# Optimization experiments

Hardware: AMD Instinct MI355X
Metric: run time of the kernel (lower is better)

Reference implementation:

```python
import jax, jax.numpy as jnp
import numpy as np
from jax import lax

B, N, H, D = 4, 384, 8, 5          # graphs, nodes/graph, heads, max multi-hop dist
NE, E_TOT, DH, L = 2048, 8192, 256, 10  # edges/graph, total real edges, d_hidden, curve samples
N_SPATIAL, N_EDGE_DIST = 64, 128


def _bn(x, g, b):
    # eval-mode BatchNorm1d (running_mean=0, running_var=1): affine only
    return x * g + b


def _conv1d(x, w):
    # x: [E, C, L], w: [O, I, 3], SAME padding, stride 1
    return lax.conv_general_dilated(x, w, (1,), 'SAME',
                                    dimension_numbers=('NCH', 'OIH', 'NCH'))


def setup_inputs() -> dict:
    key = jax.random.key(0)
    ks = iter(jax.random.split(key, 64))
    nrm = lambda shape, s=0.02: jax.random.normal(next(ks), shape, jnp.float32) * s
    std = 0.02 / np.sqrt(12.0)  # init_params with n_layer=12 for Linear weights
    inp = {}
    inp['attn_bias'] = jax.random.normal(next(ks), (B, N + 1, N + 1), jnp.float32)
    inp['spatial_pos'] = jax.random.randint(next(ks), (B, N, N), 0, N_SPATIAL)
    inp['d2_dist'] = jax.random.normal(next(ks), (B, N, N, 32), jnp.float32)
    inp['a3_dist'] = jax.random.normal(next(ks), (B, N, N, 32), jnp.float32)
    inp['edge_data'] = jax.random.normal(next(ks), (E_TOT, L, 7), jnp.float32)
    inp['edge_path'] = jax.random.randint(next(ks), (B, N, N, D), 0, NE + 1)
    inp['edge_padding_mask'] = jnp.zeros((B, NE), bool)  # all real edges
    inp['src'] = jax.random.randint(next(ks), (E_TOT,), 0, B * N)
    inp['dst'] = jax.random.randint(next(ks), (E_TOT,), 0, B * N)
    inp['node_data'] = jax.random.normal(next(ks), (B * N, DH), jnp.float32)
    # --- parameters ---
    inp['spatial_emb'] = nrm((N_SPATIAL, H)).at[0].set(0.0)  # padding_idx=0
    inp['t_virtual'] = nrm((1, H))
    inp['w_d2'] = nrm((H, 32), std); inp['b_d2'] = jnp.zeros((H,), jnp.float32)
    inp['w_a3'] = nrm((H, 32), std); inp['b_a3'] = jnp.zeros((H,), jnp.float32)
    inp['cw1'] = nrm((64, 7, 3), std);  inp['cg1'] = jnp.ones((64,));  inp['cb1'] = jnp.zeros((64,))
    inp['cw2'] = nrm((128, 64, 3), std); inp['cg2'] = jnp.ones((128,)); inp['cb2'] = jnp.zeros((128,))
    inp['cw3'] = nrm((256, 128, 3), std); inp['cg3'] = jnp.ones((256,)); inp['cb3'] = jnp.zeros((256,))
    inp['cw_out'] = nrm((H, 256), std)
    # _EdgeConv (UV-Net style): proj Linear(d_hidden->H), MLP(H->64->H), BN, GIN eps
    inp['wp'] = nrm((H, DH), std); inp['bp'] = jnp.zeros((H,))
    inp['w1'] = nrm((64, H), std); inp['b1'] = jnp.zeros((64,))
    inp['g1'] = jnp.ones((64,)); inp['bb1'] = jnp.zeros((64,))
    inp['w2'] = nrm((H, 64), std); inp['b2'] = jnp.zeros((H,))
    inp['g_out'] = jnp.ones((H,)); inp['bb_out'] = jnp.zeros((H,))
    inp['eps'] = jnp.zeros((), jnp.float32)
    inp['edge_dis_w'] = nrm((N_EDGE_DIST * H * H, 1))
    return inp


def reference(attn_bias, spatial_pos, d2_dist, a3_dist, edge_data, edge_path,
              edge_padding_mask, src, dst, node_data, spatial_emb, t_virtual,
              w_d2, b_d2, w_a3, b_a3, cw1, cg1, cb1, cw2, cg2, cb2, cw3, cg3, cb3,
              cw_out, wp, bp, w1, b1, g1, bb1, w2, b2, g_out, bb_out, eps, edge_dis_w):
    gab = jnp.repeat(attn_bias[:, None], H, axis=1)            # [B,H,N+1,N+1]
    spb = spatial_emb[spatial_pos]                              # [B,N,N,H]
    d2b = d2_dist @ w_d2.T + b_d2                               # [B,N,N,H]
    a3b = a3_dist @ w_a3.T + b_a3                               # [B,N,N,H]
    # CurveEncoder on per-edge curve samples
    x = jnp.transpose(edge_data, (0, 2, 1))                     # [E,7,L]
    x = jax.nn.leaky_relu(_bn(_conv1d(x, cw1), cg1[:, None], cb1[:, None]))
    x = jax.nn.leaky_relu(_bn(_conv1d(x, cw2), cg2[:, None], cb2[:, None]))
    x = jax.nn.leaky_relu(_bn(_conv1d(x, cw3), cg3[:, None], cb3[:, None]))
    ef = jnp.mean(x, axis=-1) @ cw_out.T                        # [E,H]
    # _EdgeConv: combine endpoint node features with edge features
    proj = node_data @ wp.T + bp                                # [B*N,H]
    h = (1.0 + eps) * ef + proj[src] + proj[dst]
    h = jax.nn.relu(_bn(h @ w1.T + b1, g1, bb1)) @ w2.T + b2
    edge_out = jax.nn.relu(_bn(h, g_out, bb_out))               # [E,H]
    # scatter real-edge features into padded table (row NE stays zero = padding)
    valid = (~edge_padding_mask).reshape(-1)                    # [B*NE]
    gidx = jnp.maximum(jnp.cumsum(valid) - 1, 0)
    vals = jnp.where(valid[:, None], edge_out[gidx], 0.0).reshape(B, NE, H)
    edge_feature = jnp.zeros((B, NE + 1, H), edge_out.dtype).at[:, :NE].set(vals)
    # gather along multi-hop paths, per-distance head mixing (bmm), normalize
    ep = edge_path.reshape(B, N * N * D)
    edge_input = jax.vmap(lambda f, p: f[p])(edge_feature, ep)  # [B,N*N*D,H]
    edge_input = edge_input.reshape(B, N, N, D, H)
    wdis = edge_dis_w.reshape(-1, H, H)[:D]                     # [D,H,H]
    edge_input = jnp.einsum('bijdh,dhk->bijdk', edge_input, wdis)
    sp = jnp.where(spatial_pos == 0, 1, spatial_pos)
    sp = jnp.where(sp > 1, sp - 1, sp)
    sp = jnp.clip(sp, 0, D)
    edge_bias = edge_input.sum(-2) / sp[..., None].astype(edge_input.dtype)
    inner = spb + d2b + a3b + edge_bias                         # [B,N,N,H]
    gab = gab.at[:, :, 1:, 1:].add(jnp.transpose(inner, (0, 3, 1, 2)))
    t = t_virtual.reshape(1, H, 1)
    gab = gab.at[:, :, 1:, 0].add(t)
    gab = gab.at[:, :, 0, :].add(t)
    return gab + attn_bias[:, None]
```

## Files before the change

kernel.cpp:

```cpp
#include <hip/hip_runtime.h>

#define NB    4
#define NNODE 384
#define NH    8
#define ND    5
#define NEDGE 2048
#define NEP1  2049
#define ETOT  8192
#define DHID  256
#define NP1   385
#define SQ1   (NP1*NP1)
#define NPOS  98304
#define NPOS2 (NPOS + 2)

typedef __attribute__((ext_vector_type(8)))  short short8;
typedef __attribute__((ext_vector_type(16))) float float16;

__device__ __forceinline__ unsigned short f2bf(float f) {
    union { float f; unsigned int u; } v; v.f = f;
    unsigned int u = v.u;
    return (unsigned short)((u + 0x7FFFu + ((u >> 16) & 1u)) >> 16);
}
__device__ __forceinline__ unsigned pkbf(float a, float b) {
    return (unsigned)f2bf(a) | ((unsigned)f2bf(b) << 16);
}
__device__ __forceinline__ short8 mk8(unsigned a, unsigned b, unsigned c, unsigned d) {
    union { unsigned u[4]; short8 s; } x; x.u[0]=a; x.u[1]=b; x.u[2]=c; x.u[3]=d; return x.s;
}
__device__ __forceinline__ float leaky(float v) { return v > 0.f ? v : 0.01f * v; }
__device__ __forceinline__ float16 zero16() {
    float16 z;
#pragma unroll
    for (int i = 0; i < 16; ++i) z[i] = 0.f;
    return z;
}
__device__ __forceinline__ void gl_lds16(const void* g, void* l) {
    __builtin_amdgcn_global_load_lds(
        (const __attribute__((address_space(1))) unsigned int*)g,
        (__attribute__((address_space(3))) unsigned int*)l,
        16, 0, 0);
}

__global__ __launch_bounds__(256) void prep_kernel(
    const float* __restrict__ cw1, const float* __restrict__ cw2, const float* __restrict__ cw3,
    const float* __restrict__ cw_out,
    const float* __restrict__ node_data, const float* __restrict__ wp, const float* __restrict__ bp,
    unsigned short* __restrict__ W1f, unsigned short* __restrict__ W2f, unsigned short* __restrict__ W3f,
    unsigned short* __restrict__ Wof,
    float* __restrict__ proj, float* __restrict__ edge_feature)
{
    int gid = blockIdx.x * 256 + threadIdx.x;
    if (gid < 98304) {
        int j = gid & 7, lane = (gid >> 3) & 63, blk = gid >> 9;
        int ks = blk & 7, tp = (blk >> 3) % 3, mt = blk / 24;
        int oc = mt * 32 + (lane & 31);
        int ic = ks * 16 + (lane >> 5) * 8 + j;
        W3f[gid] = f2bf(cw3[(oc * 128 + ic) * 3 + tp]);
    } else if (gid < 122880) {
        int f = gid - 98304;
        int j = f & 7, lane = (f >> 3) & 63, blk = f >> 9;
        int ks = blk & 3, tp = (blk >> 2) % 3, mt = blk / 12;
        int oc = mt * 32 + (lane & 31);
        int ic = ks * 16 + (lane >> 5) * 8 + j;
        W2f[f] = f2bf(cw2[(oc * 64 + ic) * 3 + tp]);
    } else if (gid < 124928) {
        int f = gid - 122880;
        int j = f & 7, lane = (f >> 3) & 63, blk = f >> 9;
        int ks = blk & 1, mt = blk >> 1;
        int oc = mt * 32 + (lane & 31);
        int k = ks * 16 + (lane >> 5) * 8 + j;
        int tp = k >> 3, c = k & 7;
        float v = (tp < 3 && c < 7) ? cw1[oc * 21 + c * 3 + tp] : 0.f;
        W1f[f] = f2bf(v);
    } else if (gid < 137216) {
        int f = gid - 124928;
        int v = f >> 3, h = f & 7;
        const float* nd = node_data + (size_t)v * DHID;
        const float* ww = wp + h * DHID;
        float acc = bp[h];
#pragma unroll 4
        for (int c = 0; c < DHID; c += 4)
            acc += nd[c]*ww[c] + nd[c+1]*ww[c+1] + nd[c+2]*ww[c+2] + nd[c+3]*ww[c+3];
        proj[f] = acc;
    } else if (gid < 137248) {
        int f = gid - 137216;
        int b = f >> 3, h = f & 7;
        edge_feature[((size_t)b * NEP1 + NEDGE) * NH + h] = 0.f;
    } else if (gid < 145440) {
        int f = gid - 137248;
        int j = f & 7, lane = (f >> 3) & 63, g = f >> 9;
        int m = lane & 31;
        int k = g * 16 + (lane >> 5) * 8 + j;
        Wof[f] = (m < 8) ? f2bf(cw_out[m * 256 + k]) : (unsigned short)0;
    }
}

#define X0_GROWS 8
__global__ __launch_bounds__(256) void pack_kernel(
    const float* __restrict__ edge_data,
    unsigned short* __restrict__ X0buf, unsigned short* __restrict__ X1buf,
    unsigned short* __restrict__ X2buf)
{
    int gid = blockIdx.x * 256 + threadIdx.x;
    const int NX0 = (NPOS + 2 * X0_GROWS) * 8;
    if (gid < NX0) {
        int row = gid >> 3, ch = gid & 7;
        int pos = row - X0_GROWS;
        unsigned short v = 0;
        if (pos >= 0 && pos < NPOS && ch < 7) {
            int pm = pos % 12;
            if (pm >= 1 && pm <= 10)
                v = f2bf(edge_data[(size_t)(pos / 12) * 70 + (pm - 1) * 7 + ch]);
        }
        X0buf[gid] = v;
    } else if (gid < NX0 + 128) {
        int f = gid - NX0;
        int p = f >> 5, rest = f & 31;
        int row = (rest >> 4) ? (NPOS + 1) : 0, col = rest & 15;
        X1buf[((size_t)p * NPOS2 + row) * 16 + col] = 0;
    } else if (gid < NX0 + 128 + 256) {
        int f = gid - NX0 - 128;
        int p = f >> 5, rest = f & 31;
        int row = (rest >> 4) ? (NPOS + 1) : 0, col = rest & 15;
        X2buf[((size_t)p * NPOS2 + row) * 16 + col] = 0;
    }
}

__global__ __launch_bounds__(256, 4) void conv1_kernel(
    const unsigned short* __restrict__ X0, const unsigned short* __restrict__ W1f,
    const float* __restrict__ cg1, const float* __restrict__ cb1,
    unsigned short* __restrict__ X1)
{
    const int t = threadIdx.x, wv = t >> 6, lane = t & 63;
    const int q = lane >> 5, n = lane & 31;
    const int pos = blockIdx.x * 128 + wv * 32 + n;

    float16 acc0 = zero16(), acc1 = zero16();
#pragma unroll
    for (int ks = 0; ks < 2; ++ks) {
        short8 b  = *(const short8*)(X0 + (pos - 1 + 2 * ks + q) * 8);
        short8 a0 = *(const short8*)(W1f + ((0 * 2 + ks) * 64 + lane) * 8);
        short8 a1 = *(const short8*)(W1f + ((1 * 2 + ks) * 64 + lane) * 8);
        acc0 = __builtin_amdgcn_mfma_f32_32x32x16_bf16(a0, b, acc0, 0, 0, 0);
        acc1 = __builtin_amdgcn_mfma_f32_32x32x16_bf16(a1, b, acc1, 0, 0, 0);
    }
    int pm = pos % 12;
    bool valid = (pm != 0) && (pm != 11);
#pragma unroll
    for (int mt = 0; mt < 2; ++mt) {
        const float16& acc = mt ? acc1 : acc0;
#pragma unroll
        for (int r2 = 0; r2 < 4; ++r2) {
            int oc0 = mt * 32 + 8 * r2 + 4 * q;
            float4 g4 = *(const float4*)(cg1 + oc0);
            float4 b4 = *(const float4*)(cb1 + oc0);
            unsigned short uu[4];
            uu[0] = valid ? f2bf(leaky(acc[r2*4+0] * g4.x + b4.x)) : (unsigned short)0;
            uu[1] = valid ? f2bf(leaky(acc[r2*4+1] * g4.y + b4.y)) : (unsigned short)0;
            uu[2] = valid ? f2bf(leaky(acc[r2*4+2] * g4.z + b4.z)) : (unsigned short)0;
            uu[3] = valid ? f2bf(leaky(acc[r2*4+3] * g4.w + b4.w)) : (unsigned short)0;
            uint2 pk; pk.x = uu[0] | ((unsigned)uu[1] << 16); pk.y = uu[2] | ((unsigned)uu[3] << 16);
            *(uint2*)(void*)(X1 + ((size_t)(oc0 >> 4) * NPOS2 + pos + 1) * 16 + (oc0 & 15)) = pk;
        }
    }
}

__global__ __launch_bounds__(256, 3) void conv2_kernel(
    const unsigned short* __restrict__ X1, const unsigned short* __restrict__ W2f,
    const float* __restrict__ cg2, const float* __restrict__ cb2,
    unsigned short* __restrict__ X2)
{
    __shared__ __align__(16) unsigned short sB[2][1568];
    const int t = threadIdx.x, wv = t >> 6, lane = t & 63;
    const int q = lane >> 5, n = lane & 31;
    const int base = blockIdx.x * 96;
    const int cbase = (wv < 3) ? wv * 64 : 132;

    gl_lds16(X1 + ((size_t)0 * NPOS2 + base) * 16 + (cbase + lane) * 8,
             &sB[0][cbase * 8]);

    float16 acc[3];
#pragma unroll
    for (int nt = 0; nt < 3; ++nt) acc[nt] = zero16();

    __syncthreads();

#pragma unroll
    for (int ks = 0; ks < 4; ++ks) {
        if (ks < 3)
            gl_lds16(X1 + ((size_t)(ks + 1) * NPOS2 + base) * 16 + (cbase + lane) * 8,
                     &sB[(ks + 1) & 1][cbase * 8]);
        const unsigned short* bb = sB[ks & 1];
#pragma unroll
        for (int tp = 0; tp < 3; ++tp) {
            short8 a = *(const short8*)(W2f + (((wv * 3 + tp) * 4 + ks) * 64 + lane) * 8);
#pragma unroll
            for (int nt = 0; nt < 3; ++nt) {
                short8 b = *(const short8*)(bb + (nt * 32 + n + tp) * 16 + q * 8);
                acc[nt] = __builtin_amdgcn_mfma_f32_32x32x16_bf16(a, b, acc[nt], 0, 0, 0);
            }
        }
        __syncthreads();
    }

#pragma unroll
    for (int nt = 0; nt < 3; ++nt) {
        int pos = base + nt * 32 + n;
        int pm = pos % 12;
        bool valid = (pm != 0) && (pm != 11);
#pragma unroll
        for (int r2 = 0; r2 < 4; ++r2) {
            int oc0 = wv * 32 + 8 * r2 + 4 * q;
            float4 g4 = *(const float4*)(cg2 + oc0);
            float4 b4 = *(const float4*)(cb2 + oc0);
            unsigned short uu[4];
            uu[0] = valid ? f2bf(leaky(acc[nt][r2*4+0] * g4.x + b4.x)) : (unsigned short)0;
            uu[1] = valid ? f2bf(leaky(acc[nt][r2*4+1] * g4.y + b4.y)) : (unsigned short)0;
            uu[2] = valid ? f2bf(leaky(acc[nt][r2*4+2] * g4.z + b4.z)) : (unsigned short)0;
            uu[3] = valid ? f2bf(leaky(acc[nt][r2*4+3] * g4.w + b4.w)) : (unsigned short)0;
            uint2 pk; pk.x = uu[0] | ((unsigned)uu[1] << 16); pk.y = uu[2] | ((unsigned)uu[3] << 16);
            *(uint2*)(void*)(X2 + ((size_t)(oc0 >> 4) * NPOS2 + pos + 1) * 16 + (oc0 & 15)) = pk;
        }
    }
}

__global__ __launch_bounds__(256, 2) void conv3_kernel(
    const unsigned short* __restrict__ X2, const unsigned short* __restrict__ W3f,
    const unsigned short* __restrict__ Wof,
    const float* __restrict__ cg3, const float* __restrict__ cb3,
    const int* __restrict__ src, const int* __restrict__ dst,
    const float* __restrict__ w1, const float* __restrict__ b1,
    const float* __restrict__ g1, const float* __restrict__ bb1,
    const float* __restrict__ w2, const float* __restrict__ b2,
    const float* __restrict__ g_out, const float* __restrict__ bb_out,
    const float* __restrict__ eps, const float* __restrict__ proj,
    float* __restrict__ edge_feature)
{
    __shared__ float fs[3072 + 64 + 512];
    __shared__ __align__(16) unsigned short sB[2][1568];
    const int t = threadIdx.x, wv = t >> 6, lane = t & 63;
    const int q = lane >> 5, n = lane & 31;
    const int base = blockIdx.x * 96;
    const int cbase = (wv < 3) ? wv * 64 : 132;

    gl_lds16(X2 + ((size_t)0 * NPOS2 + base) * 16 + (cbase + lane) * 8,
             &sB[0][cbase * 8]);

    float16 acc[2][3];
#pragma unroll
    for (int i = 0; i < 2; ++i)
#pragma unroll
        for (int nt = 0; nt < 3; ++nt) acc[i][nt] = zero16();

    __syncthreads();

#pragma unroll
    for (int ks = 0; ks < 8; ++ks) {
        if (ks < 7)
            gl_lds16(X2 + ((size_t)(ks + 1) * NPOS2 + base) * 16 + (cbase + lane) * 8,
                     &sB[(ks + 1) & 1][cbase * 8]);
        const unsigned short* bb = sB[ks & 1];
#pragma unroll
        for (int tp = 0; tp < 3; ++tp) {
            short8 a0 = *(const short8*)(W3f + ((((wv*2+0) * 3 + tp) * 8 + ks) * 64 + lane) * 8);
            short8 a1 = *(const short8*)(W3f + ((((wv*2+1) * 3 + tp) * 8 + ks) * 64 + lane) * 8);
#pragma unroll
            for (int nt = 0; nt < 3; ++nt) {
                short8 b = *(const short8*)(bb + (nt * 32 + n + tp) * 16 + q * 8);
                acc[0][nt] = __builtin_amdgcn_mfma_f32_32x32x16_bf16(a0, b, acc[0][nt], 0, 0, 0);
                acc[1][nt] = __builtin_amdgcn_mfma_f32_32x32x16_bf16(a1, b, acc[1][nt], 0, 0, 0);
            }
        }
        __syncthreads();
    }

    short8 wof[4];
#pragma unroll
    for (int g = 0; g < 4; ++g)
        wof[g] = *(const short8*)(Wof + ((wv * 4 + g) * 64 + lane) * 8);

#pragma unroll
    for (int nt = 0; nt < 3; ++nt) {
        int pm = (nt * 32 + n) % 12;
        bool valid = (pm != 0) && (pm != 11);
        float16 p = zero16();
#pragma unroll
        for (int i = 0; i < 2; ++i) {
            int mt = wv * 2 + i;
            float av[16];
#pragma unroll
            for (int r2 = 0; r2 < 4; ++r2) {
                int oc0 = mt * 32 + 8 * r2 + 4 * q;
                float4 g4 = *(const float4*)(cg3 + oc0);
                float4 b4 = *(const float4*)(cb3 + oc0);
                av[r2*4+0] = valid ? leaky(acc[i][nt][r2*4+0] * g4.x + b4.x) : 0.f;
                av[r2*4+1] = valid ? leaky(acc[i][nt][r2*4+1] * g4.y + b4.y) : 0.f;
                av[r2*4+2] = valid ? leaky(acc[i][nt][r2*4+2] * g4.z + b4.z) : 0.f;
                av[r2*4+3] = valid ? leaky(acc[i][nt][r2*4+3] * g4.w + b4.w) : 0.f;
            }
            unsigned pk[8], op[8];
#pragma unroll
            for (int z = 0; z < 8; ++z) pk[z] = pkbf(av[2*z], av[2*z+1]);
#pragma unroll
            for (int z = 0; z < 8; ++z) op[z] = __shfl_xor((int)pk[z], 32);
            short8 f0 = q == 0 ? mk8(pk[0], pk[1], op[0], op[1])
                               : mk8(op[2], op[3], pk[2], pk[3]);
            short8 f1 = q == 0 ? mk8(pk[4], pk[5], op[4], op[5])
                               : mk8(op[6], op[7], pk[6], pk[7]);
            p = __builtin_amdgcn_mfma_f32_32x32x16_bf16(wof[i*2+0], f0, p, 0, 0, 0);
            p = __builtin_amdgcn_mfma_f32_32x32x16_bf16(wof[i*2+1], f1, p, 0, 0, 0);
        }
        float4 st = make_float4(p[0], p[1], p[2], p[3]);
        *(float4*)&fs[((wv * 96) + nt * 32 + n) * 8 + 4 * q] = st;
    }
    __syncthreads();

    if (t < 64) {
        int e = t >> 3, h = t & 7;
        float s = 0.f;
#pragma unroll
        for (int w = 0; w < 4; ++w)
#pragma unroll 4
            for (int l = 0; l < 12; ++l) s += fs[(w * 96 + e * 12 + l) * 8 + h];
        float efv = 0.1f * s;
        int ge = blockIdx.x * 8 + e;
        fs[3072 + e * 8 + h] = (1.f + eps[0]) * efv
                             + proj[src[ge] * NH + h] + proj[dst[ge] * NH + h];
    }
    __syncthreads();

#pragma unroll
    for (int bb = 0; bb < 512; bb += 256) {
        int idx = bb + t;
        int e = idx >> 6, o = idx & 63;
        float a = b1[o];
#pragma unroll
        for (int h = 0; h < 8; ++h) a += fs[3072 + e * 8 + h] * w1[o * 8 + h];
        float v = a * g1[o] + bb1[o];
        fs[3136 + e * 64 + o] = v > 0.f ? v : 0.f;
    }
    __syncthreads();

    if (t < 64) {
        int e = t >> 3, h = t & 7;
        float a = b2[h];
#pragma unroll 8
        for (int o = 0; o < 64; ++o) a += fs[3136 + e * 64 + o] * w2[h * 64 + o];
        float v = a * g_out[h] + bb_out[h];
        v = v > 0.f ? v : 0.f;
        int ge = blockIdx.x * 8 + e;
        int b = ge >> 11, el2 = ge & (NEDGE - 1);
        edge_feature[((size_t)b * NEP1 + el2) * NH + h] = v;
    }
}

__global__ __launch_bounds__(256) void tbl_kernel(
    const float* __restrict__ edge_feature, const float* __restrict__ edge_dis_w,
    float* __restrict__ T)
{
    int idx = blockIdx.x * 256 + threadIdx.x;
    if (idx >= NEP1 * 8) return;
    int pi = idx >> 3, k = idx & 7;
    int d = blockIdx.y, b = blockIdx.z;
    const float* ef = edge_feature + ((size_t)b * NEP1 + pi) * NH;
    const float* w  = edge_dis_w + d * 64 + k;
    float s = 0.f;
#pragma unroll
    for (int h = 0; h < 8; ++h) s += ef[h] * w[h * 8];
    T[(((size_t)b * ND + d) * NEP1 + pi) * 8 + k] = s;
}

__global__ __launch_bounds__(256) void bias_kernel(
    const float* __restrict__ attn_bias, const int* __restrict__ spatial_pos,
    const float* __restrict__ d2_dist, const float* __restrict__ a3_dist,
    const int* __restrict__ edge_path,
    const float* __restrict__ spatial_emb, const float* __restrict__ t_virtual,
    const float* __restrict__ w_d2, const float* __restrict__ b_d2,
    const float* __restrict__ w_a3, const float* __restrict__ b_a3,
    const float* __restrict__ Tbl,
    float* __restrict__ out)
{
    __shared__ __align__(16) float s_emb[512];
    __shared__ __align__(16) float s_wd2[256];
    __shared__ __align__(16) float s_wa3[256];
    __shared__ float s_t[8], s_bd2[8], s_ba3[8];

    int t = threadIdx.x;
    for (int i = t; i < 512; i += 256) s_emb[i] = spatial_emb[i];
    if (t < 256) { s_wd2[t] = w_d2[t]; s_wa3[t] = w_a3[t]; }
    if (t < 8) { s_t[t] = t_virtual[t]; s_bd2[t] = b_d2[t]; s_ba3[t] = b_a3[t]; }
    __syncthreads();

    int gc = blockIdx.x * 32 + (t >> 3);
    int part = t & 7;
    if (gc >= NB * SQ1) return;
    int b   = gc / SQ1;
    int rem = gc % SQ1;
    int i = rem / NP1, j = rem % NP1;

    float base = 2.f * attn_bias[gc];
    bool border = (i == 0) || (j == 0);
    int r = border ? 0 : i - 1, c = border ? 0 : j - 1;
    size_t nidx = ((size_t)b * NNODE + r) * NNODE + c;
    int sp = spatial_pos[nidx];

    float acc[8];
    {
        float4 vd = ((const float4*)(d2_dist + nidx * 32))[part];
        float4 va = ((const float4*)(a3_dist + nidx * 32))[part];
        const float4* wd2 = (const float4*)s_wd2;
        const float4* wa3 = (const float4*)s_wa3;
#pragma unroll
        for (int h = 0; h < 8; ++h) {
            float4 w4 = wd2[h * 8 + part];
            float4 v4 = wa3[h * 8 + part];
            acc[h] = vd.x*w4.x + vd.y*w4.y + vd.z*w4.z + vd.w*w4.w
                   + va.x*v4.x + va.y*v4.y + va.z*v4.z + va.w*v4.w;
        }
    }

    float edp = 0.f;
    const int* ep = edge_path + nidx * ND;
    const float* Tb = Tbl + (size_t)b * (ND * NEP1 * 8);
#pragma unroll
    for (int d = 0; d < ND; ++d) {
        int pi = ep[d];
        edp += Tb[((size_t)d * NEP1 + pi) * 8 + part];
    }
    int spd = (sp == 0) ? 1 : sp;
    spd = (spd > 1) ? spd - 1 : spd;
    spd = (spd > ND) ? ND : spd;
    float inv = 1.f / (float)spd;

#pragma unroll
    for (int m = 1; m < 8; m <<= 1) {
#pragma unroll
        for (int h = 0; h < 8; ++h) acc[h] += __shfl_xor(acc[h], m, 64);
    }

    float val = border ? (base + s_t[part])
                       : (base + acc[part] + edp * inv
                          + s_emb[sp * 8 + part] + s_bd2[part] + s_ba3[part]);
    out[((size_t)b * NH + part) * SQ1 + (size_t)i * NP1 + j] = val;
}

extern "C" void kernel_launch(void* const* d_in, const int* in_sizes, int n_in,
                              void* d_out, int out_size, void* d_ws, size_t ws_size,
                              hipStream_t stream)
{
    const float* attn_bias   = (const float*)d_in[0];
    const int*   spatial_pos = (const int*)  d_in[1];
    const float* d2_dist     = (const float*)d_in[2];
    const float* a3_dist     = (const float*)d_in[3];
    const float* edge_data   = (const float*)d_in[4];
    const int*   edge_path   = (const int*)  d_in[5];
    const int*   src         = (const int*)  d_in[7];
    const int*   dst         = (const int*)  d_in[8];
    const float* node_data   = (const float*)d_in[9];
    const float* spatial_emb = (const float*)d_in[10];
    const float* t_virtual   = (const float*)d_in[11];
    const float* w_d2        = (const float*)d_in[12];
    const float* b_d2        = (const float*)d_in[13];
    const float* w_a3        = (const float*)d_in[14];
    const float* b_a3        = (const float*)d_in[15];
    const float* cw1         = (const float*)d_in[16];
    const float* cg1         = (const float*)d_in[17];
    const float* cb1         = (const float*)d_in[18];
    const float* cw2         = (const float*)d_in[19];
    const float* cg2         = (const float*)d_in[20];
    const float* cb2         = (const float*)d_in[21];
    const float* cw3         = (const float*)d_in[22];
    const float* cg3         = (const float*)d_in[23];
    const float* cb3         = (const float*)d_in[24];
    const float* cw_out      = (const float*)d_in[25];
    const float* wp          = (const float*)d_in[26];
    const float* bp          = (const float*)d_in[27];
    const float* w1          = (const float*)d_in[28];
    const float* b1          = (const float*)d_in[29];
    const float* g1          = (const float*)d_in[30];
    const float* bb1         = (const float*)d_in[31];
    const float* w2          = (const float*)d_in[32];
    const float* b2          = (const float*)d_in[33];
    const float* g_out       = (const float*)d_in[34];
    const float* bb_out      = (const float*)d_in[35];
    const float* eps         = (const float*)d_in[36];
    const float* edge_dis_w  = (const float*)d_in[37];

    float*          proj  = (float*)d_ws;
    float*          ef    = proj + NB * NNODE * NH;
    unsigned short* W1f   = (unsigned short*)(ef + NB * NEP1 * NH);
    unsigned short* W2f   = W1f + 2048;
    unsigned short* W3f   = W2f + 24576;
    unsigned short* Wof   = W3f + 98304;
    unsigned short* X0buf = Wof + 8192;
    unsigned short* X1buf = X0buf + (size_t)(NPOS + 2 * X0_GROWS) * 8;
    unsigned short* X2buf = X1buf + (size_t)4 * NPOS2 * 16;
    unsigned short* X0 = X0buf + X0_GROWS * 8;
    float*          Tbl   = (float*)X0buf;

    prep_kernel<<<569, 256, 0, stream>>>(cw1, cw2, cw3, cw_out, node_data, wp, bp,
                                         W1f, W2f, W3f, Wof, proj, ef);
    pack_kernel<<<3074, 256, 0, stream>>>(edge_data, X0buf, X1buf, X2buf);

    conv1_kernel<<<NPOS / 128, 256, 0, stream>>>(X0, W1f, cg1, cb1, X1buf);
    conv2_kernel<<<NPOS / 96, 256, 0, stream>>>(X1buf, W2f, cg2, cb2, X2buf);
    conv3_kernel<<<NPOS / 96, 256, 0, stream>>>(X2buf, W3f, Wof, cg3, cb3,
                                                src, dst, w1, b1, g1, bb1,
                                                w2, b2, g_out, bb_out, eps,
                                                proj, ef);

    dim3 tgrid((NEP1 * 8 + 255) / 256, ND, NB);
    tbl_kernel<<<tgrid, 256, 0, stream>>>(ef, edge_dis_w, Tbl);

    int nbias = (NB * SQ1 * 8 + 255) / 256;
    bias_kernel<<<nbias, 256, 0, stream>>>(
        attn_bias, spatial_pos, d2_dist, a3_dist, edge_path,
        spatial_emb, t_virtual, w_d2, b_d2, w_a3, b_a3,
        Tbl, (float*)d_out);
}
```

Measured before the change: 355.6 us.

## Preload all conv K-slices to LDS, vectorize projection, restructure bias kernel with transpose-reduce

In conv2 and conv3, every K-slice of the input tile is loaded into shared memory up front, which removes the per-step double-buffer barriers at the cost of larger LDS use and possibly lower occupancy. The node projection dot product now uses float4 loads with four independent accumulators. The bias kernel handles several cell groups per thread across loop iterations, two at a time to expose more memory-level parallelism. Its butterfly shuffle reduction over eight heads becomes a transpose-style reduce that needs fewer shuffles, and it launches 8x fewer blocks.

```diff
diff --git a/kernel.cpp b/kernel.cpp
--- a/kernel.cpp
+++ b/kernel.cpp
@@ -75,13 +75,21 @@
     } else if (gid < 137216) {
         int f = gid - 124928;
         int v = f >> 3, h = f & 7;
-        const float* nd = node_data + (size_t)v * DHID;
-        const float* ww = wp + h * DHID;
-        float acc = bp[h];
+        const float4* nd4 = (const float4*)(node_data + (size_t)v * DHID);
+        const float4* ww4 = (const float4*)(wp + (size_t)h * DHID);
+        float s0 = 0.f, s1 = 0.f, s2 = 0.f, s3 = 0.f;
 #pragma unroll 4
-        for (int c = 0; c < DHID; c += 4)
-            acc += nd[c]*ww[c] + nd[c+1]*ww[c+1] + nd[c+2]*ww[c+2] + nd[c+3]*ww[c+3];
-        proj[f] = acc;
+        for (int c = 0; c < 64; c += 4) {
+            float4 x0 = nd4[c+0], y0 = ww4[c+0];
+            float4 x1 = nd4[c+1], y1 = ww4[c+1];
+            float4 x2 = nd4[c+2], y2 = ww4[c+2];
+            float4 x3 = nd4[c+3], y3 = ww4[c+3];
+            s0 += x0.x*y0.x + x0.y*y0.y + x0.z*y0.z + x0.w*y0.w;
+            s1 += x1.x*y1.x + x1.y*y1.y + x1.z*y1.z + x1.w*y1.w;
+            s2 += x2.x*y2.x + x2.y*y2.y + x2.z*y2.z + x2.w*y2.w;
+            s3 += x3.x*y3.x + x3.y*y3.y + x3.z*y3.z + x3.w*y3.w;
+        }
+        proj[f] = bp[h] + (s0 + s1) + (s2 + s3);
     } else if (gid < 137248) {
         int f = gid - 137216;
         int b = f >> 3, h = f & 7;
@@ -170,14 +178,16 @@
     const float* __restrict__ cg2, const float* __restrict__ cb2,
     unsigned short* __restrict__ X2)
 {
-    __shared__ __align__(16) unsigned short sB[2][1568];
+    __shared__ __align__(16) unsigned short sB[4][1568];
     const int t = threadIdx.x, wv = t >> 6, lane = t & 63;
     const int q = lane >> 5, n = lane & 31;
     const int base = blockIdx.x * 96;
     const int cbase = (wv < 3) ? wv * 64 : 132;
 
-    gl_lds16(X1 + ((size_t)0 * NPOS2 + base) * 16 + (cbase + lane) * 8,
-             &sB[0][cbase * 8]);
+#pragma unroll
+    for (int ks = 0; ks < 4; ++ks)
+        gl_lds16(X1 + ((size_t)ks * NPOS2 + base) * 16 + (cbase + lane) * 8,
+                 &sB[ks][cbase * 8]);
 
     float16 acc[3];
 #pragma unroll
@@ -186,22 +196,16 @@
     __syncthreads();
 
 #pragma unroll
-    for (int ks = 0; ks < 4; ++ks) {
-        if (ks < 3)
-            gl_lds16(X1 + ((size_t)(ks + 1) * NPOS2 + base) * 16 + (cbase + lane) * 8,
-                     &sB[(ks + 1) & 1][cbase * 8]);
-        const unsigned short* bb = sB[ks & 1];
+    for (int ks = 0; ks < 4; ++ks)
 #pragma unroll
         for (int tp = 0; tp < 3; ++tp) {
             short8 a = *(const short8*)(W2f + (((wv * 3 + tp) * 4 + ks) * 64 + lane) * 8);
 #pragma unroll
             for (int nt = 0; nt < 3; ++nt) {
-                short8 b = *(const short8*)(bb + (nt * 32 + n + tp) * 16 + q * 8);
+                short8 b = *(const short8*)(&sB[ks][(nt * 32 + n + tp) * 16 + q * 8]);
                 acc[nt] = __builtin_amdgcn_mfma_f32_32x32x16_bf16(a, b, acc[nt], 0, 0, 0);
             }
         }
-        __syncthreads();
-    }
 
 #pragma unroll
     for (int nt = 0; nt < 3; ++nt) {
@@ -237,14 +241,16 @@
     float* __restrict__ edge_feature)
 {
     __shared__ float fs[3072 + 64 + 512];
-    __shared__ __align__(16) unsigned short sB[2][1568];
+    __shared__ __align__(16) unsigned short sB[8][1568];
     const int t = threadIdx.x, wv = t >> 6, lane = t & 63;
     const int q = lane >> 5, n = lane & 31;
     const int base = blockIdx.x * 96;
     const int cbase = (wv < 3) ? wv * 64 : 132;
 
-    gl_lds16(X2 + ((size_t)0 * NPOS2 + base) * 16 + (cbase + lane) * 8,
-             &sB[0][cbase * 8]);
+#pragma unroll
+    for (int ks = 0; ks < 8; ++ks)
+        gl_lds16(X2 + ((size_t)ks * NPOS2 + base) * 16 + (cbase + lane) * 8,
+                 &sB[ks][cbase * 8]);
 
     float16 acc[2][3];
 #pragma unroll
@@ -255,24 +261,18 @@
     __syncthreads();
 
 #pragma unroll
-    for (int ks = 0; ks < 8; ++ks) {
-        if (ks < 7)
-            gl_lds16(X2 + ((size_t)(ks + 1) * NPOS2 + base) * 16 + (cbase + lane) * 8,
-                     &sB[(ks + 1) & 1][cbase * 8]);
-        const unsigned short* bb = sB[ks & 1];
+    for (int ks = 0; ks < 8; ++ks)
 #pragma unroll
         for (int tp = 0; tp < 3; ++tp) {
             short8 a0 = *(const short8*)(W3f + ((((wv*2+0) * 3 + tp) * 8 + ks) * 64 + lane) * 8);
             short8 a1 = *(const short8*)(W3f + ((((wv*2+1) * 3 + tp) * 8 + ks) * 64 + lane) * 8);
 #pragma unroll
             for (int nt = 0; nt < 3; ++nt) {
-                short8 b = *(const short8*)(bb + (nt * 32 + n + tp) * 16 + q * 8);
+                short8 b = *(const short8*)(&sB[ks][(nt * 32 + n + tp) * 16 + q * 8]);
                 acc[0][nt] = __builtin_amdgcn_mfma_f32_32x32x16_bf16(a0, b, acc[0][nt], 0, 0, 0);
                 acc[1][nt] = __builtin_amdgcn_mfma_f32_32x32x16_bf16(a1, b, acc[1][nt], 0, 0, 0);
             }
         }
-        __syncthreads();
-    }
 
     short8 wof[4];
 #pragma unroll
@@ -387,61 +387,87 @@
 
     int t = threadIdx.x;
     for (int i = t; i < 512; i += 256) s_emb[i] = spatial_emb[i];
-    if (t < 256) { s_wd2[t] = w_d2[t]; s_wa3[t] = w_a3[t]; }
+    s_wd2[t] = w_d2[t]; s_wa3[t] = w_a3[t];
     if (t < 8) { s_t[t] = t_virtual[t]; s_bd2[t] = b_d2[t]; s_ba3[t] = b_a3[t]; }
     __syncthreads();
 
-    int gc = blockIdx.x * 32 + (t >> 3);
-    int part = t & 7;
-    if (gc >= NB * SQ1) return;
-    int b   = gc / SQ1;
-    int rem = gc % SQ1;
-    int i = rem / NP1, j = rem % NP1;
-
-    float base = 2.f * attn_bias[gc];
-    bool border = (i == 0) || (j == 0);
-    int r = border ? 0 : i - 1, c = border ? 0 : j - 1;
-    size_t nidx = ((size_t)b * NNODE + r) * NNODE + c;
-    int sp = spatial_pos[nidx];
-
-    float acc[8];
-    {
-        float4 vd = ((const float4*)(d2_dist + nidx * 32))[part];
-        float4 va = ((const float4*)(a3_dist + nidx * 32))[part];
-        const float4* wd2 = (const float4*)s_wd2;
-        const float4* wa3 = (const float4*)s_wa3;
+    const int part = t & 7, grp = t >> 3;
+    const bool pb0 = part & 1, pb1 = (part >> 1) & 1, pb2 = (part >> 2) & 1;
+    const float tpart = s_t[part], bd2 = s_bd2[part], ba3 = s_ba3[part];
+
+#pragma unroll 1
+    for (int it = 0; it < 4; ++it) {
+        int gbase = (blockIdx.x * 4 + it) * 64 + grp;
+
+        float basev[2]; int spv[2]; size_t nidx[2];
+        bool bord[2], valid[2];
+        float4 vd[2], va[2];
+        int bidx[2], ii[2], jj[2];
+#pragma unroll
+        for (int u = 0; u < 2; ++u) {
+            int g = gbase + 32 * u;
+            valid[u] = g < NB * SQ1;
+            if (!valid[u]) g = 0;
+            int b = g / SQ1, rem = g % SQ1;
+            int i = rem / NP1, j = rem % NP1;
+            bidx[u] = b; ii[u] = i; jj[u] = j;
+            basev[u] = 2.f * attn_bias[g];
+            bool border = (i == 0) || (j == 0);
+            bord[u] = border;
+            int r = border ? 0 : i - 1, c = border ? 0 : j - 1;
+            size_t nx = ((size_t)b * NNODE + r) * NNODE + c;
+            nidx[u] = nx;
+            spv[u] = spatial_pos[nx];
+            vd[u] = ((const float4*)(d2_dist + nx * 32))[part];
+            va[u] = ((const float4*)(a3_dist + nx * 32))[part];
+        }
+
+        float edp[2];
+#pragma unroll
+        for (int u = 0; u < 2; ++u) {
+            const int* ep = edge_path + nidx[u] * ND;
+            const float* Tb = Tbl + (size_t)bidx[u] * (ND * NEP1 * 8);
+            float e = 0.f;
+#pragma unroll
+            for (int d = 0; d < ND; ++d)
+                e += Tb[((size_t)d * NEP1 + ep[d]) * 8 + part];
+            edp[u] = e;
+        }
+
+        float acc[2][8];
 #pragma unroll
         for (int h = 0; h < 8; ++h) {
-            float4 w4 = wd2[h * 8 + part];
-            float4 v4 = wa3[h * 8 + part];
-            acc[h] = vd.x*w4.x + vd.y*w4.y + vd.z*w4.z + vd.w*w4.w
-                   + va.x*v4.x + va.y*v4.y + va.z*v4.z + va.w*v4.w;
-        }
-    }
-
-    float edp = 0.f;
-    const int* ep = edge_path + nidx * ND;
-    const float* Tb = Tbl + (size_t)b * (ND * NEP1 * 8);
-#pragma unroll
-    for (int d = 0; d < ND; ++d) {
-        int pi = ep[d];
-        edp += Tb[((size_t)d * NEP1 + pi) * 8 + part];
-    }
-    int spd = (sp == 0) ? 1 : sp;
-    spd = (spd > 1) ? spd - 1 : spd;
-    spd = (spd > ND) ? ND : spd;
-    float inv = 1.f / (float)spd;
-
-#pragma unroll
-    for (int m = 1; m < 8; m <<= 1) {
-#pragma unroll
-        for (int h = 0; h < 8; ++h) acc[h] += __shfl_xor(acc[h], m, 64);
-    }
-
-    float val = border ? (base + s_t[part])
-                       : (base + acc[part] + edp * inv
-                          + s_emb[sp * 8 + part] + s_bd2[part] + s_ba3[part]);
-    out[((size_t)b * NH + part) * SQ1 + (size_t)i * NP1 + j] = val;
+            float4 w4 = ((const float4*)s_wd2)[h * 8 + part];
+            float4 v4 = ((const float4*)s_wa3)[h * 8 + part];
+#pragma unroll
+            for (int u = 0; u < 2; ++u)
+                acc[u][h] = vd[u].x*w4.x + vd[u].y*w4.y + vd[u].z*w4.z + vd[u].w*w4.w
+                          + va[u].x*v4.x + va[u].y*v4.y + va[u].z*v4.z + va[u].w*v4.w;
+        }
+
+#pragma unroll
+        for (int u = 0; u < 2; ++u) {
+            float y0 = (pb0 ? acc[u][1] : acc[u][0]) + __shfl_xor(pb0 ? acc[u][0] : acc[u][1], 1, 64);
+            float y1 = (pb0 ? acc[u][3] : acc[u][2]) + __shfl_xor(pb0 ? acc[u][2] : acc[u][3], 1, 64);
+            float y2 = (pb0 ? acc[u][5] : acc[u][4]) + __shfl_xor(pb0 ? acc[u][4] : acc[u][5], 1, 64);
+            float y3 = (pb0 ? acc[u][7] : acc[u][6]) + __shfl_xor(pb0 ? acc[u][6] : acc[u][7], 1, 64);
+            float z0 = (pb1 ? y1 : y0) + __shfl_xor(pb1 ? y0 : y1, 2, 64);
+            float z1 = (pb1 ? y3 : y2) + __shfl_xor(pb1 ? y2 : y3, 2, 64);
+            float rr = (pb2 ? z1 : z0) + __shfl_xor(pb2 ? z0 : z1, 4, 64);
+
+            int sp = spv[u];
+            int spd = (sp == 0) ? 1 : sp;
+            spd = (spd > 1) ? spd - 1 : spd;
+            spd = (spd > ND) ? ND : spd;
+            float inv = 1.f / (float)spd;
+
+            float val = bord[u] ? (basev[u] + tpart)
+                                : (basev[u] + rr + edp[u] * inv
+                                   + s_emb[sp * 8 + part] + bd2 + ba3);
+            if (valid[u])
+                out[((size_t)bidx[u] * NH + part) * SQ1 + (size_t)ii[u] * NP1 + jj[u]] = val;
+        }
+    }
 }
 
 extern "C" void kernel_launch(void* const* d_in, const int* in_sizes, int n_in,
@@ -512,7 +538,7 @@
     dim3 tgrid((NEP1 * 8 + 255) / 256, ND, NB);
     tbl_kernel<<<tgrid, 256, 0, stream>>>(ef, edge_dis_w, Tbl);
 
-    int nbias = (NB * SQ1 * 8 + 255) / 256;
+    int nbias = (NB * SQ1 + 255) / 256;
     bias_kernel<<<nbias, 256, 0, stream>>>(
         attn_bias, spatial_pos, d2_dist, a3_dist, edge_path,
         spatial_emb, t_virtual, w_d2, b_d2, w_a3, b_a3,
```

Result: no change. 353.8 us (-0.5%).
